# Kernel tuning notes

Measured on AMD Instinct MI355X. Metric: run time of the kernel, lower is better.

## Reference

```python
import jax, jax.numpy as jnp
import numpy as np

VOXEL_SIZE = 0.4
STRIDE = 2
NUM_BATCH = 4
PRE_MAXSIZE = 1024  # nms_premaxsize
NMS_THR = 0.1
NEG_INF = -1e9


def setup_inputs() -> dict:
    key = jax.random.key(0)
    ks = jax.random.split(key, 7)
    N, C = 200000, 256
    feat = jax.random.normal(ks[0], (N, C), dtype=jnp.float32)
    batch_idx = jax.random.randint(ks[1], (N,), 0, NUM_BATCH, dtype=jnp.int32)
    coor = jax.random.randint(ks[2], (N, 2), 0, 400, dtype=jnp.int32)
    W_cls = jax.random.normal(ks[3], (C, 2), dtype=jnp.float32) * 0.02
    b_cls = jnp.zeros((2,), dtype=jnp.float32)
    W_reg = jax.random.normal(ks[4], (C, 9), dtype=jnp.float32) * 0.02
    b_reg = jnp.zeros((9,), dtype=jnp.float32)
    return {"feat": feat, "batch_idx": batch_idx, "coor": coor,
            "W_cls": W_cls, "b_cls": b_cls, "W_reg": W_reg, "b_reg": b_reg}


def _bev_iou(bx):
    # bx: [K,7] (x,y,z,l,w,h,r); axis-aligned BEV IoU on (x,y,l,w)
    x, y, l, w = bx[:, 0], bx[:, 1], bx[:, 3], bx[:, 4]
    x1, x2 = x - l / 2, x + l / 2
    y1, y2 = y - w / 2, y + w / 2
    ix = jnp.maximum(jnp.minimum(x2[:, None], x2[None, :]) - jnp.maximum(x1[:, None], x1[None, :]), 0.0)
    iy = jnp.maximum(jnp.minimum(y2[:, None], y2[None, :]) - jnp.maximum(y1[:, None], y1[None, :]), 0.0)
    inter = ix * iy
    area = l * w
    union = area[:, None] + area[None, :] - inter
    return inter / jnp.maximum(union, 1e-6)


def _nms_keep(iou):
    # greedy NMS over score-descending rows; returns keep mask [K]
    K = iou.shape[0]
    idx = jnp.arange(K)

    def body(i, supp):
        keep_i = jnp.logical_not(supp[i])
        new = keep_i & (iou[i] > NMS_THR) & (idx > i)
        return supp | new

    supp = jax.lax.fori_loop(0, K, body, jnp.zeros((K,), dtype=bool))
    return jnp.logical_not(supp)


def reference(feat, batch_idx, coor, W_cls, b_cls, W_reg, b_reg):
    # ---- shared heads over all sparse voxels ----
    cls_logits = feat @ W_cls + b_cls            # [N, 1+1] (neg evidence, class)
    probs = jax.nn.softmax(cls_logits, axis=-1)
    cls_prob = probs[:, 1:]                      # [N, n_cls]
    conf = jnp.max(cls_prob, axis=-1)            # [N]
    label = jnp.argmax(cls_prob, axis=-1)        # [N]

    reg = feat @ W_reg + b_reg                   # [N, 9] -> ctr(3) dim(3) dir(2) scr(1)
    ctr, dim, drn, scr = reg[:, :3], reg[:, 3:6], reg[:, 6:8], reg[:, 8]
    scr = jax.nn.sigmoid(scr)                    # sigmoid_keys=['scr']

    # indices2metric: voxel indices -> metric centers
    centers = coor.astype(jnp.float32) * (VOXEL_SIZE * STRIDE)  # [N, 2]

    xy = centers + ctr[:, :2]
    z = ctr[:, 2]
    lwh = jnp.exp(jnp.clip(dim, -6.0, 6.0))
    angle = jnp.arctan2(drn[:, 0], drn[:, 1])
    boxes = jnp.concatenate([xy, z[:, None], lwh, angle[:, None]], axis=-1)  # [N, 7]
    score = conf * scr                           # [N]

    def per_sample(b):
        s = jnp.where(batch_idx == b, score, NEG_INF)
        vals, idx = jax.lax.top_k(s, PRE_MAXSIZE)          # score-sorted (desc)
        bx = boxes[idx]                                     # [K, 7]
        lb = label[idx]                                     # [K]
        valid = vals > NEG_INF / 2
        iou = _bev_iou(bx)
        keep = _nms_keep(iou) & valid
        out = jnp.concatenate([bx, vals[:, None]], axis=-1) * keep[:, None]  # [K, 8]
        return out, lb, keep

    out, lb, keep = jax.vmap(per_sample)(jnp.arange(NUM_BATCH))
    return out, lb, keep
```

## Files before the change

### kernel.cpp

```cpp
#include <hip/hip_runtime.h>
#include <math.h>

#define NBATCH 4
#define PRE 1024
#define CAND 4096
#define NHIST 65536
#define MAXSLOT 384

__device__ __forceinline__ unsigned long long allow_mask(int i, int l) {
    int base = l << 6;
    if (i < base) return ~0ull;
    int sh = i - base + 1;
    if (sh >= 64) return 0ull;
    return (~0ull) << sh;
}

__global__ void k0_weights(const float* __restrict__ Wcls, const float* __restrict__ bcls,
                           const float* __restrict__ Wreg, const float* __restrict__ breg,
                           double* __restrict__ Wd3, float* __restrict__ Wf8,
                           double* __restrict__ biasD, float* __restrict__ biasF) {
    int j = blockIdx.x;
    int c = threadIdx.x;
    if (j < 2) {
        Wd3[j * 256 + c] = (double)Wcls[c * 2 + j];
        if (c == 0) biasD[j] = (double)bcls[j];
    } else if (j == 10) {
        Wd3[2 * 256 + c] = (double)Wreg[c * 9 + 8];
        if (c == 0) biasD[2] = (double)breg[8];
    } else {
        int r = j - 2;
        Wf8[r * 256 + c] = Wreg[c * 9 + r];
        if (c == 0) biasF[r] = breg[r];
    }
}

__global__ __launch_bounds__(256) void k1_points(
    const float* __restrict__ feat, const int* __restrict__ batch_idx,
    const int* __restrict__ coor, const double* __restrict__ Wd3,
    const float* __restrict__ Wf8, const double* __restrict__ biasD,
    const float* __restrict__ biasF, float* __restrict__ pointData,
    unsigned long long* __restrict__ keys, unsigned int* __restrict__ hist, int N) {
    const int gp = blockIdx.x * 256 + threadIdx.x;
    if (gp >= N) return;
    const float4* fp = (const float4*)(feat + (size_t)gp * 256);

    double accD0 = 0.0, accD1 = 0.0, accD2 = 0.0;
    float accF[8];
#pragma unroll
    for (int j = 0; j < 8; ++j) accF[j] = 0.f;

#pragma unroll 2
    for (int it = 0; it < 8; ++it) {
        float4 v[8];
#pragma unroll
        for (int j = 0; j < 8; ++j) v[j] = fp[it * 8 + j];
#pragma unroll
        for (int j = 0; j < 8; ++j) {
            const int c = it * 32 + j * 4;
            const float vv[4] = {v[j].x, v[j].y, v[j].z, v[j].w};
#pragma unroll
            for (int m = 0; m < 4; ++m) {
                const double fd = (double)vv[m];
                accD0 = fma(fd, Wd3[c + m], accD0);
                accD1 = fma(fd, Wd3[256 + c + m], accD1);
                accD2 = fma(fd, Wd3[512 + c + m], accD2);
#pragma unroll
                for (int jj = 0; jj < 8; ++jj)
                    accF[jj] = fmaf(vv[m], Wf8[jj * 256 + c + m], accF[jj]);
            }
        }
    }

    double d0 = biasD[0] + accD0, d1 = biasD[1] + accD1, d2 = biasD[2] + accD2;
    float f[8];
#pragma unroll
    for (int j = 0; j < 8; ++j) f[j] = biasF[j] + accF[j];
    double conf = 1.0 / (1.0 + exp(-(d1 - d0)));
    double scr = 1.0 / (1.0 + exp(-d2));
    double score = conf * scr;
    float s32 = (float)score;

    float cx = (float)coor[2 * gp] * 0.8f;
    float cy = (float)coor[2 * gp + 1] * 0.8f;
    float bx = cx + f[0], by = cy + f[1], bz = f[2];
    float bl = expf(fminf(fmaxf(f[3], -6.f), 6.f));
    float bw = expf(fminf(fmaxf(f[4], -6.f), 6.f));
    float bh = expf(fminf(fmaxf(f[5], -6.f), 6.f));
    float ba = atan2f(f[6], f[7]);

    float4* pd = (float4*)(pointData + (size_t)gp * 8);
    pd[0] = make_float4(bx, by, bz, bl);
    pd[1] = make_float4(bw, bh, ba, s32);
    keys[gp] = (unsigned long long)__double_as_longlong(score);
    int b = batch_idx[gp];
    atomicAdd(&hist[b * NHIST + (__float_as_uint(s32) >> 16)], 1u);
}

__global__ __launch_bounds__(256) void k2_thresh(const unsigned int* __restrict__ hist,
                                                 unsigned int* __restrict__ Tarr) {
    int b = blockIdx.x, tid = threadIdx.x;
    __shared__ unsigned int csum[256];
    __shared__ unsigned int chunkv[256];
    __shared__ int stc;
    __shared__ unsigned int scum;
    const unsigned int* h = hist + b * NHIST;
    unsigned int s = 0;
    for (int m = 0; m < 256; ++m) s += h[tid * 256 + m];
    csum[tid] = s;
    __syncthreads();
    if (tid == 0) {
        unsigned int cum = 0; int tc = -1;
        for (int t = 255; t >= 0; --t) {
            if (cum + csum[t] >= 1024u) { tc = t; break; }
            cum += csum[t];
        }
        stc = tc; scum = cum;
    }
    __syncthreads();
    int tc = stc;
    if (tc < 0) { if (tid == 0) Tarr[b] = 0u; return; }
    chunkv[tid] = h[tc * 256 + tid];
    __syncthreads();
    if (tid == 0) {
        unsigned int cum = scum, T = (unsigned int)(tc * 256);
        for (int m = 255; m >= 0; --m) {
            unsigned int c = chunkv[m];
            if (cum + c >= 1024u) { T = (unsigned int)(tc * 256 + m); break; }
            cum += c;
        }
        Tarr[b] = T;
    }
}

__global__ void k3_compact(const int* __restrict__ batch_idx, const float* __restrict__ pointData,
                           const unsigned long long* __restrict__ keys,
                           const unsigned int* __restrict__ Tarr, unsigned int* __restrict__ candCount,
                           unsigned int* __restrict__ candIdx, unsigned long long* __restrict__ candKey,
                           int N) {
    int p = blockIdx.x * 256 + threadIdx.x;
    if (p >= N) return;
    int b = batch_idx[p];
    float s32 = pointData[(size_t)p * 8 + 7];
    unsigned int bucket = __float_as_uint(s32) >> 16;
    if (bucket >= Tarr[b]) {
        unsigned int pos = atomicAdd(&candCount[b], 1u);
        if (pos < CAND) {
            candIdx[b * CAND + pos] = (unsigned int)p;
            candKey[b * CAND + pos] = keys[p];
        }
    }
}

__global__ __launch_bounds__(1024) void k4_sort(const unsigned int* __restrict__ candCount,
                                                const unsigned int* __restrict__ candIdx,
                                                const unsigned long long* __restrict__ candKey,
                                                const float* __restrict__ pointData,
                                                float* __restrict__ topBox,
                                                unsigned int* __restrict__ validArr) {
    int b = blockIdx.x, tid = threadIdx.x;
    __shared__ unsigned long long ka[CAND];
    __shared__ unsigned int id[CAND];
    unsigned int cnt = candCount[b];
    if (cnt > CAND) cnt = CAND;
    int n = (cnt <= 2048u) ? 2048 : 4096;
    for (int t = tid; t < n; t += 1024) {
        if ((unsigned int)t < cnt) {
            ka[t] = ~candKey[b * CAND + t];
            id[t] = candIdx[b * CAND + t];
        } else {
            ka[t] = ~0ull;
            id[t] = 0xFFFFFFFFu;
        }
    }
    __syncthreads();
    for (int k = 2; k <= n; k <<= 1) {
        for (int j = k >> 1; j > 0; j >>= 1) {
            for (int t = tid; t < n; t += 1024) {
                int l = t ^ j;
                if (l > t) {
                    bool up = ((t & k) == 0);
                    unsigned long long kt = ka[t], kl = ka[l];
                    unsigned int it_ = id[t], il = id[l];
                    bool gt = (kt > kl) || (kt == kl && it_ > il);
                    if (gt == up) { ka[t] = kl; ka[l] = kt; id[t] = il; id[l] = it_; }
                }
            }
            __syncthreads();
        }
    }
    unsigned int gi = id[tid];
    bool valid = (gi != 0xFFFFFFFFu) && ((unsigned int)tid < cnt);
    float v[8];
#pragma unroll
    for (int k = 0; k < 8; ++k) v[k] = 0.f;
    if (valid) {
        const float* pd = pointData + (size_t)gi * 8;
#pragma unroll
        for (int k = 0; k < 8; ++k) v[k] = pd[k];
    }
    float* tb = topBox + (size_t)(b * PRE + tid) * 8;
#pragma unroll
    for (int k = 0; k < 8; ++k) tb[k] = v[k];
    validArr[b * PRE + tid] = valid ? 1u : 0u;
}

__global__ __launch_bounds__(256) void k5_iou(const float* __restrict__ topBox,
                                              unsigned long long* __restrict__ M) {
    int wid = blockIdx.x * 4 + (threadIdx.x >> 6);
    int lane = threadIdx.x & 63;
    int b = wid >> 14;
    int rem = wid & 16383;
    int i = rem >> 4;
    int wj = rem & 15;
    if (wj < (i >> 6)) return;
    const float* bi = topBox + (size_t)(b * PRE + i) * 8;
    int j = wj * 64 + lane;
    const float* bj = topBox + (size_t)(b * PRE + j) * 8;
    float xi = bi[0], yi = bi[1], li = bi[3], wi_ = bi[4];
    float xj = bj[0], yj = bj[1], lj = bj[3], wj_ = bj[4];
    float x1i = xi - li * 0.5f, x2i = xi + li * 0.5f;
    float y1i = yi - wi_ * 0.5f, y2i = yi + wi_ * 0.5f;
    float x1j = xj - lj * 0.5f, x2j = xj + lj * 0.5f;
    float y1j = yj - wj_ * 0.5f, y2j = yj + wj_ * 0.5f;
    float ix = fmaxf(fminf(x2i, x2j) - fmaxf(x1i, x1j), 0.0f);
    float iy = fmaxf(fminf(y2i, y2j) - fmaxf(y1i, y1j), 0.0f);
    float inter = ix * iy;
    float ai = li * wi_, aj = lj * wj_;
    float uni = ai + aj - inter;
    float iou = inter / fmaxf(uni, 1e-6f);
    unsigned long long m = __ballot(iou > 0.1f);
    if (lane == 0) M[(size_t)(b * PRE + i) * 16 + wj] = m;
}

__global__ __launch_bounds__(256) void k6_nms(const unsigned long long* __restrict__ M,
                                              const unsigned int* __restrict__ validArr,
                                              const float* __restrict__ topBox,
                                              float* __restrict__ out0,
                                              float* __restrict__ keepOut) {
    __shared__ unsigned long long Mc[MAXSLOT * 16];
    __shared__ unsigned int slotIdx[PRE];
    __shared__ unsigned int cntSh;
    __shared__ unsigned long long suppSh[16];
    int b = blockIdx.x, tid = threadIdx.x;
    if (tid == 0) cntSh = 0;
    __syncthreads();
    for (int r = tid; r < PRE; r += 256) {
        const unsigned long long* row = M + (size_t)(b * PRE + r) * 16;
        unsigned long long w[16];
        unsigned long long o = 0ull;
#pragma unroll
        for (int l = 0; l < 16; ++l) { w[l] = row[l] & allow_mask(r, l); o |= w[l]; }
        unsigned int s = 0xFFFFFFFFu;
        if (o != 0ull) {
            unsigned int slot = atomicAdd(&cntSh, 1u);
            if (slot < MAXSLOT) {
                s = slot;
#pragma unroll
                for (int l = 0; l < 16; ++l) Mc[slot * 16 + l] = w[l];
            } else s = 0xFFFFFFFEu;
        }
        slotIdx[r] = s;
    }
    __syncthreads();
    if (tid < 64) {
        int lane = tid;
        unsigned long long supp = 0ull;
        for (int g = 0; g < 16; ++g) {
            unsigned long long act = __ballot(slotIdx[g * 64 + lane] != 0xFFFFFFFFu);
            while (act) {
                int bit = __builtin_ctzll(act);
                act &= act - 1ull;
                int i = g * 64 + bit;
                unsigned long long wsup = __shfl(supp, g);
                bool keep_i = ((wsup >> (i & 63)) & 1ull) == 0ull;
                if (keep_i && lane < 16) {
                    unsigned int s = slotIdx[i];
                    unsigned long long add = (s < MAXSLOT)
                        ? Mc[s * 16 + lane]
                        : (M[(size_t)(b * PRE + i) * 16 + lane] & allow_mask(i, lane));
                    supp |= add;
                }
            }
        }
        if (lane < 16) suppSh[lane] = supp;
    }
    __syncthreads();
    for (int r = tid; r < PRE; r += 256) {
        bool keep = (((suppSh[r >> 6] >> (r & 63)) & 1ull) == 0ull) && (validArr[b * PRE + r] != 0u);
        float kf = keep ? 1.0f : 0.0f;
        const float* tb = topBox + (size_t)(b * PRE + r) * 8;
        float* o = out0 + (size_t)(b * PRE + r) * 8;
#pragma unroll
        for (int k = 0; k < 8; ++k) o[k] = tb[k] * kf;
        keepOut[b * PRE + r] = kf;
    }
}

extern "C" void kernel_launch(void* const* d_in, const int* in_sizes, int n_in,
                              void* d_out, int out_size, void* d_ws, size_t ws_size,
                              hipStream_t stream) {
    int N = in_sizes[0] / 256;
    const float* feat = (const float*)d_in[0];
    const int* batch_idx = (const int*)d_in[1];
    const int* coor = (const int*)d_in[2];
    const float* Wcls = (const float*)d_in[3];
    const float* bcls = (const float*)d_in[4];
    const float* Wreg = (const float*)d_in[5];
    const float* breg = (const float*)d_in[6];

    char* ws = (char*)d_ws;
    size_t off = 0;
    auto take = [&](size_t bytes) -> char* {
        char* r = ws + off;
        off += (bytes + 255) & ~(size_t)255;
        return r;
    };
    float* pointData = (float*)take((size_t)N * 8 * 4);
    unsigned long long* keys = (unsigned long long*)take((size_t)N * 8);
    unsigned int* hist = (unsigned int*)take((size_t)NBATCH * NHIST * 4);
    unsigned int* candCount = (unsigned int*)take(NBATCH * 4);
    unsigned int* Tarr = (unsigned int*)take(NBATCH * 4);
    unsigned int* candIdx = (unsigned int*)take(NBATCH * CAND * 4);
    unsigned long long* candKey = (unsigned long long*)take(NBATCH * CAND * 8);
    float* topBox = (float*)take(NBATCH * PRE * 8 * 4);
    unsigned int* validArr = (unsigned int*)take(NBATCH * PRE * 4);
    unsigned long long* M = (unsigned long long*)take((size_t)NBATCH * PRE * 16 * 8);
    double* Wd3 = (double*)take(3 * 256 * 8);
    float* Wf8 = (float*)take(8 * 256 * 4);
    double* biasD = (double*)take(3 * 8);
    float* biasF = (float*)take(8 * 4);

    float* out0 = (float*)d_out;
    float* keepOut = out0 + NBATCH * PRE * 8 + NBATCH * PRE;

    hipMemsetAsync(d_out, 0, (size_t)out_size * 4, stream);
    hipMemsetAsync(hist, 0, (size_t)NBATCH * NHIST * 4 + NBATCH * 4, stream);

    int pbPts = (N + 255) / 256;
    k0_weights<<<dim3(11), dim3(256), 0, stream>>>(Wcls, bcls, Wreg, breg, Wd3, Wf8, biasD, biasF);
    k1_points<<<dim3(pbPts), dim3(256), 0, stream>>>(feat, batch_idx, coor,
                                                     Wd3, Wf8, biasD, biasF,
                                                     pointData, keys, hist, N);
    k2_thresh<<<dim3(NBATCH), dim3(256), 0, stream>>>(hist, Tarr);
    k3_compact<<<dim3(pbPts), dim3(256), 0, stream>>>(batch_idx, pointData, keys, Tarr,
                                                      candCount, candIdx, candKey, N);
    k4_sort<<<dim3(NBATCH), dim3(1024), 0, stream>>>(candCount, candIdx, candKey,
                                                     pointData, topBox, validArr);
    k5_iou<<<dim3(NBATCH * PRE * 16 / 4), dim3(256), 0, stream>>>(topBox, M);
    k6_nms<<<dim3(NBATCH), dim3(256), 0, stream>>>(M, validArr, topBox, out0, keepOut);
}
```

Baseline: 488.8 us.

## Pack float score and index into one sort key and software-pipeline feature loads

The double-precision score key array is dropped. Candidates now carry a single 64-bit key holding the inverted float32 score bits and the point index, so the bitonic sort moves one shared array with a single comparison. The point kernel double-buffers its feature loads with a sched barrier and asks for higher occupancy through launch bounds. Ranking on float32 scores instead of double may change the order when scores tie at float precision. Forcing 4 blocks per CU may also cause register spills.

```diff
diff --git a/kernel.cpp b/kernel.cpp
--- a/kernel.cpp
+++ b/kernel.cpp
@@ -34,12 +34,12 @@
     }
 }
 
-__global__ __launch_bounds__(256) void k1_points(
+__global__ __launch_bounds__(256, 4) void k1_points(
     const float* __restrict__ feat, const int* __restrict__ batch_idx,
     const int* __restrict__ coor, const double* __restrict__ Wd3,
     const float* __restrict__ Wf8, const double* __restrict__ biasD,
     const float* __restrict__ biasF, float* __restrict__ pointData,
-    unsigned long long* __restrict__ keys, unsigned int* __restrict__ hist, int N) {
+    unsigned int* __restrict__ hist, int N) {
     const int gp = blockIdx.x * 256 + threadIdx.x;
     if (gp >= N) return;
     const float4* fp = (const float4*)(feat + (size_t)gp * 256);
@@ -49,11 +49,17 @@
 #pragma unroll
     for (int j = 0; j < 8; ++j) accF[j] = 0.f;
 
-#pragma unroll 2
-    for (int it = 0; it < 8; ++it) {
-        float4 v[8];
-#pragma unroll
-        for (int j = 0; j < 8; ++j) v[j] = fp[it * 8 + j];
+    float4 va[8], vb[8];
+
+    auto LOAD_A = [&](int it) {
+#pragma unroll
+        for (int j = 0; j < 8; ++j) va[j] = fp[it * 8 + j];
+    };
+    auto LOAD_B = [&](int it) {
+#pragma unroll
+        for (int j = 0; j < 8; ++j) vb[j] = fp[it * 8 + j];
+    };
+    auto COMP = [&](const float4 (&v)[8], int it) {
 #pragma unroll
         for (int j = 0; j < 8; ++j) {
             const int c = it * 32 + j * 4;
@@ -69,6 +75,16 @@
                     accF[jj] = fmaf(vv[m], Wf8[jj * 256 + c + m], accF[jj]);
             }
         }
+    };
+
+    LOAD_A(0);
+#pragma unroll
+    for (int it = 0; it < 8; ++it) {
+        if (it < 7) {
+            if (it & 1) LOAD_A(it + 1); else LOAD_B(it + 1);
+        }
+        __builtin_amdgcn_sched_barrier(0);
+        if (it & 1) COMP(vb, it); else COMP(va, it);
     }
 
     double d0 = biasD[0] + accD0, d1 = biasD[1] + accD1, d2 = biasD[2] + accD2;
@@ -91,7 +107,6 @@
     float4* pd = (float4*)(pointData + (size_t)gp * 8);
     pd[0] = make_float4(bx, by, bz, bl);
     pd[1] = make_float4(bw, bh, ba, s32);
-    keys[gp] = (unsigned long long)__double_as_longlong(score);
     int b = batch_idx[gp];
     atomicAdd(&hist[b * NHIST + (__float_as_uint(s32) >> 16)], 1u);
 }
@@ -133,45 +148,33 @@
 }
 
 __global__ void k3_compact(const int* __restrict__ batch_idx, const float* __restrict__ pointData,
-                           const unsigned long long* __restrict__ keys,
                            const unsigned int* __restrict__ Tarr, unsigned int* __restrict__ candCount,
-                           unsigned int* __restrict__ candIdx, unsigned long long* __restrict__ candKey,
-                           int N) {
+                           unsigned long long* __restrict__ candKey, int N) {
     int p = blockIdx.x * 256 + threadIdx.x;
     if (p >= N) return;
     int b = batch_idx[p];
     float s32 = pointData[(size_t)p * 8 + 7];
-    unsigned int bucket = __float_as_uint(s32) >> 16;
-    if (bucket >= Tarr[b]) {
+    unsigned int sb = __float_as_uint(s32);
+    if ((sb >> 16) >= Tarr[b]) {
         unsigned int pos = atomicAdd(&candCount[b], 1u);
         if (pos < CAND) {
-            candIdx[b * CAND + pos] = (unsigned int)p;
-            candKey[b * CAND + pos] = keys[p];
+            candKey[b * CAND + pos] = ((unsigned long long)(~sb) << 32) | (unsigned int)p;
         }
     }
 }
 
 __global__ __launch_bounds__(1024) void k4_sort(const unsigned int* __restrict__ candCount,
-                                                const unsigned int* __restrict__ candIdx,
                                                 const unsigned long long* __restrict__ candKey,
                                                 const float* __restrict__ pointData,
                                                 float* __restrict__ topBox,
                                                 unsigned int* __restrict__ validArr) {
     int b = blockIdx.x, tid = threadIdx.x;
     __shared__ unsigned long long ka[CAND];
-    __shared__ unsigned int id[CAND];
     unsigned int cnt = candCount[b];
     if (cnt > CAND) cnt = CAND;
     int n = (cnt <= 2048u) ? 2048 : 4096;
-    for (int t = tid; t < n; t += 1024) {
-        if ((unsigned int)t < cnt) {
-            ka[t] = ~candKey[b * CAND + t];
-            id[t] = candIdx[b * CAND + t];
-        } else {
-            ka[t] = ~0ull;
-            id[t] = 0xFFFFFFFFu;
-        }
-    }
+    for (int t = tid; t < n; t += 1024)
+        ka[t] = ((unsigned int)t < cnt) ? candKey[b * CAND + t] : ~0ull;
     __syncthreads();
     for (int k = 2; k <= n; k <<= 1) {
         for (int j = k >> 1; j > 0; j >>= 1) {
@@ -180,16 +183,15 @@
                 if (l > t) {
                     bool up = ((t & k) == 0);
                     unsigned long long kt = ka[t], kl = ka[l];
-                    unsigned int it_ = id[t], il = id[l];
-                    bool gt = (kt > kl) || (kt == kl && it_ > il);
-                    if (gt == up) { ka[t] = kl; ka[l] = kt; id[t] = il; id[l] = it_; }
+                    if ((kt > kl) == up) { ka[t] = kl; ka[l] = kt; }
                 }
             }
             __syncthreads();
         }
     }
-    unsigned int gi = id[tid];
-    bool valid = (gi != 0xFFFFFFFFu) && ((unsigned int)tid < cnt);
+    unsigned long long kt = ka[tid];
+    unsigned int gi = (unsigned int)kt;
+    bool valid = ((unsigned int)tid < cnt) && (gi != 0xFFFFFFFFu);
     float v[8];
 #pragma unroll
     for (int k = 0; k < 8; ++k) v[k] = 0.f;
@@ -316,11 +318,9 @@
         return r;
     };
     float* pointData = (float*)take((size_t)N * 8 * 4);
-    unsigned long long* keys = (unsigned long long*)take((size_t)N * 8);
     unsigned int* hist = (unsigned int*)take((size_t)NBATCH * NHIST * 4);
     unsigned int* candCount = (unsigned int*)take(NBATCH * 4);
     unsigned int* Tarr = (unsigned int*)take(NBATCH * 4);
-    unsigned int* candIdx = (unsigned int*)take(NBATCH * CAND * 4);
     unsigned long long* candKey = (unsigned long long*)take(NBATCH * CAND * 8);
     float* topBox = (float*)take(NBATCH * PRE * 8 * 4);
     unsigned int* validArr = (unsigned int*)take(NBATCH * PRE * 4);
@@ -340,11 +340,11 @@
     k0_weights<<<dim3(11), dim3(256), 0, stream>>>(Wcls, bcls, Wreg, breg, Wd3, Wf8, biasD, biasF);
     k1_points<<<dim3(pbPts), dim3(256), 0, stream>>>(feat, batch_idx, coor,
                                                      Wd3, Wf8, biasD, biasF,
-                                                     pointData, keys, hist, N);
+                                                     pointData, hist, N);
     k2_thresh<<<dim3(NBATCH), dim3(256), 0, stream>>>(hist, Tarr);
-    k3_compact<<<dim3(pbPts), dim3(256), 0, stream>>>(batch_idx, pointData, keys, Tarr,
-                                                      candCount, candIdx, candKey, N);
-    k4_sort<<<dim3(NBATCH), dim3(1024), 0, stream>>>(candCount, candIdx, candKey,
+    k3_compact<<<dim3(pbPts), dim3(256), 0, stream>>>(batch_idx, pointData, Tarr,
+                                                      candCount, candKey, N);
+    k4_sort<<<dim3(NBATCH), dim3(1024), 0, stream>>>(candCount, candKey,
                                                      pointData, topBox, validArr);
     k5_iou<<<dim3(NBATCH * PRE * 16 / 4), dim3(256), 0, stream>>>(topBox, M);
     k6_nms<<<dim3(NBATCH), dim3(256), 0, stream>>>(M, validArr, topBox, out0, keepOut);
```

Result: faster. 459.4 us (-6.0%).
